# Optimization experiments

Measured on AMD Instinct MI355X. Metric: run time of the kernel, lower is better.

## Reference

```python
import jax, jax.numpy as jnp
import numpy as np

B, T, F_IN = 64, 396, 128
D_MODEL, N_HEAD, D_QKV, D_FF = 768, 8, 96, 3072
N_LAYERS, N_OUT, REL_D = 6, 256, 100


def setup_inputs():
    key = jax.random.key(0)
    cnt = [0]
    def rn(shape, std=1.0):
        cnt[0] += 1
        return jax.random.normal(jax.random.fold_in(key, cnt[0]), shape, jnp.float32) * std
    inp = {"x_raw": rn((B, T, F_IN))}
    def add_rb(p, cin, cout):
        inp[p + "_c1_w"] = rn((cout, cin, 3), (2.0 / (cin * 3)) ** 0.5)
        inp[p + "_c1_b"] = rn((cout,), 0.01)
        inp[p + "_bn1_s"] = 1.0 + rn((cout,), 0.1)
        inp[p + "_bn1_b"] = rn((cout,), 0.1)
        inp[p + "_c2_w"] = rn((cout, cout, 3), (2.0 / (cout * 3)) ** 0.5)
        inp[p + "_c2_b"] = rn((cout,), 0.01)
        inp[p + "_bn2_s"] = 1.0 + rn((cout,), 0.1)
        inp[p + "_bn2_b"] = rn((cout,), 0.1)
        inp[p + "_cr_w"] = rn((cout, cin, 1), (2.0 / cin) ** 0.5)
        inp[p + "_cr_b"] = rn((cout,), 0.01)
        inp[p + "_bnr_s"] = 1.0 + rn((cout,), 0.1)
        inp[p + "_bnr_b"] = rn((cout,), 0.1)
    add_rb("rb1", F_IN, D_MODEL)
    add_rb("rb2", D_MODEL, D_MODEL)
    inp["w_in_w"] = rn((D_MODEL, D_MODEL), D_MODEL ** -0.5)
    inp["w_in_b"] = rn((D_MODEL,), 0.01)
    inp["cls_token"] = jnp.zeros((1, 1, D_MODEL), jnp.float32)
    xav = (2.0 / (D_MODEL + D_QKV)) ** 0.5
    inp["wq"] = rn((N_LAYERS, N_HEAD, D_MODEL, D_QKV), xav)
    inp["wk"] = rn((N_LAYERS, N_HEAD, D_MODEL, D_QKV), xav)
    inp["wv"] = rn((N_LAYERS, N_HEAD, D_MODEL, D_QKV), xav)
    inp["wo"] = rn((N_LAYERS, N_HEAD, D_QKV, D_MODEL), xav)
    inp["rel_emb"] = rn((N_LAYERS, N_HEAD, 2 * REL_D + 1, D_QKV), D_QKV ** -0.5)
    inp["ln1_g"] = jnp.ones((N_LAYERS, D_MODEL), jnp.float32)
    inp["ln1_b"] = jnp.zeros((N_LAYERS, D_MODEL), jnp.float32)
    inp["ln2_g"] = jnp.ones((N_LAYERS, D_MODEL), jnp.float32)
    inp["ln2_b"] = jnp.zeros((N_LAYERS, D_MODEL), jnp.float32)
    inp["ff1_w"] = rn((N_LAYERS, D_FF, D_MODEL), (2.0 / D_MODEL) ** 0.5)
    inp["ff1_b"] = rn((N_LAYERS, D_FF), 0.01)
    inp["ff2_w"] = rn((N_LAYERS, D_MODEL, D_FF), (1.0 / D_FF) ** 0.5)
    inp["ff2_b"] = rn((N_LAYERS, D_MODEL), 0.01)
    inp["w_out_w"] = rn((N_OUT, D_MODEL), D_MODEL ** -0.5)
    inp["w_out_b"] = rn((N_OUT,), 0.01)
    return inp


def _conv1d(x, w, b, stride=1):
    # x: [B, Cin, T], w: [Cout, Cin, K]
    pad = (w.shape[-1] - 1) // 2
    y = jax.lax.conv_general_dilated(x, w, (stride,), [(pad, pad)],
                                     dimension_numbers=("NCH", "OIH", "NCH"))
    return y + b[None, :, None]


def _bn(x, s, b):
    # eval-mode BatchNorm1d folded into per-channel affine
    return x * s[None, :, None] + b[None, :, None]


def _resblock(x, c1w, c1b, s1, b1, c2w, c2b, s2, b2, crw, crb, sr, br, stride):
    h = jax.nn.relu(_bn(_conv1d(x, c1w, c1b, stride), s1, b1))
    h = _bn(_conv1d(h, c2w, c2b), s2, b2)
    r = _bn(_conv1d(x, crw, crb, stride), sr, br)
    return jax.nn.relu(h + r)


def _layer_norm(x, g, b, eps=1e-5):
    m = jnp.mean(x, -1, keepdims=True)
    v = jnp.mean((x - m) ** 2, -1, keepdims=True)
    return (x - m) * jax.lax.rsqrt(v + eps) * g + b


def _attention(x, wq, wk, wv, wo, rel):
    # x: [B, L, D]; relative-positional attention (fairseq LearnedRelativePositionalEmbedding, unmasked)
    L = x.shape[1]
    q = jnp.einsum("btf,hfa->bhta", x, wq) * (D_QKV ** -0.5)
    k = jnp.einsum("btf,hfa->bhta", x, wk)
    v = jnp.einsum("btf,hfa->bhta", x, wv)
    logits = jnp.einsum("bhqa,bhka->bhqk", q, k)
    # narrow embeddings to the 2L-1 relative positions used (L <= REL_D)
    start = REL_D - L
    rel_used = rel[:, start:start + 2 * L - 1, :]  # [h, 2L-1, a]
    pos_all = jnp.einsum("bhqa,hma->bhqm", q, rel_used)  # [B,h,L,2L-1]
    idx = jnp.arange(L)[None, :] - jnp.arange(L)[:, None] + (L - 1)  # [L,L], rel->abs skew
    logits = logits + jnp.take_along_axis(pos_all, idx[None, None], axis=3)
    probs = jax.nn.softmax(logits, axis=-1)
    o = jnp.einsum("bhqk,bhka->bhqa", probs, v)
    return jnp.einsum("bhta,haf->btf", o, wo)


def reference(x_raw, rb1_c1_w, rb1_c1_b, rb1_bn1_s, rb1_bn1_b, rb1_c2_w, rb1_c2_b, rb1_bn2_s, rb1_bn2_b, rb1_cr_w, rb1_cr_b, rb1_bnr_s, rb1_bnr_b, rb2_c1_w, rb2_c1_b, rb2_bn1_s, rb2_bn1_b, rb2_c2_w, rb2_c2_b, rb2_bn2_s, rb2_bn2_b, rb2_cr_w, rb2_cr_b, rb2_bnr_s, rb2_bnr_b, w_in_w, w_in_b, cls_token, wq, wk, wv, wo, rel_emb, ln1_g, ln1_b, ln2_g, ln2_b, ff1_w, ff1_b, ff2_w, ff2_b, w_out_w, w_out_b):
    x = jnp.transpose(x_raw, (0, 2, 1))  # [B, F_IN, T]
    x = _resblock(x, rb1_c1_w, rb1_c1_b, rb1_bn1_s, rb1_bn1_b, rb1_c2_w, rb1_c2_b, rb1_bn2_s, rb1_bn2_b, rb1_cr_w, rb1_cr_b, rb1_bnr_s, rb1_bnr_b, 2)
    x = _resblock(x, rb2_c1_w, rb2_c1_b, rb2_bn1_s, rb2_bn1_b, rb2_c2_w, rb2_c2_b, rb2_bn2_s, rb2_bn2_b, rb2_cr_w, rb2_cr_b, rb2_bnr_s, rb2_bnr_b, 2)
    x = jnp.transpose(x, (0, 2, 1))  # [B, T', D]
    x = x @ w_in_w.T + w_in_b
    cls = jnp.broadcast_to(cls_token, (x.shape[0], 1, D_MODEL))
    x = jnp.concatenate([cls, x], axis=1)  # [B, L, D], L = T'+1
    for l in range(N_LAYERS):
        a = _attention(x, wq[l], wk[l], wv[l], wo[l], rel_emb[l])
        x = _layer_norm(x + a, ln1_g[l], ln1_b[l])
        h = jax.nn.relu(x @ ff1_w[l].T + ff1_b[l]) @ ff2_w[l].T + ff2_b[l]
        x = _layer_norm(x + h, ln2_g[l], ln2_b[l])
    return x[:, 0, :] @ w_out_w.T + w_out_b
```

## Files before the change

kernel.cpp:

```cpp
#include <hip/hip_runtime.h>

typedef _Float16 h8 __attribute__((ext_vector_type(8)));
typedef float f4 __attribute__((ext_vector_type(4)));

namespace {

constexpr int DM   = 768;
constexpr int NHEAD= 8;
constexpr int DQ   = 96;
constexpr int DFF  = 3072;
constexpr int NL   = 6;
constexpr int B_   = 64;
constexpr int T0   = 396, T1 = 198, T2 = 99;
constexpr int FIN  = 128;
constexpr int L_   = 100;
constexpr int MSEQ = B_ * L_;
constexpr int M1   = B_ * T1;
constexpr int M2   = B_ * T2;
constexpr int NREL = 201;
constexpr int POSN = 256;
constexpr int RELK = 128;

enum { EPI_F32 = 0, EPI_RELU_H, EPI_H, EPI_CONV_F32, EPI_CONV_RELU_H, EPI_CONV_ADD_RELU_H };

__device__ __forceinline__ void g2l16(const _Float16* g, _Float16* l)
{
    __builtin_amdgcn_global_load_lds(
        (const __attribute__((address_space(1))) unsigned int*)g,
        (__attribute__((address_space(3))) unsigned int*)l,
        16, 0, 0);
}

template<bool CONV, int EPI, bool OPAD, int MI>
__global__ __launch_bounds__(256)
void gemm5_k(const _Float16* __restrict__ A, const _Float16* __restrict__ B,
             float* __restrict__ Cf, _Float16* __restrict__ Ch,
             const float* __restrict__ bias, const float* __restrict__ bns,
             const float* __restrict__ bnb, const float* __restrict__ res,
             int M, int N, int K, int lda,
             int T_out, int Tp_in, int stride_t, int KS, int in_off,
             int gx, int gxy,
             size_t a_z, size_t b_z, size_t c_z)
{
    constexpr int TM = MI * 32;
    __shared__ _Float16 As[TM * 64];
    __shared__ _Float16 Bs[128 * 64];

    const unsigned nwg = gridDim.x, orig = blockIdx.x;
    const unsigned q = nwg >> 3, rr_ = nwg & 7;
    const unsigned xcd = orig & 7, idx = orig >> 3;
    const unsigned wgid = (xcd < rr_) ? xcd * (q + 1) + idx
                                      : rr_ * (q + 1) + (xcd - rr_) * q + idx;
    const int bz  = (int)(wgid / (unsigned)gxy);
    const int rem = (int)(wgid - (unsigned)bz * (unsigned)gxy);
    const int by  = rem / gx;
    const int bx  = rem - by * gx;

    A += (size_t)bz * a_z;
    B += (size_t)bz * b_z;

    const int tid  = threadIdx.x;
    const int lane = tid & 63;
    const int wid  = tid >> 6;
    const int m0   = by * TM;
    const int n0   = bx * 128;
    const int wm   = (wid >> 1) * (MI * 16);
    const int wn   = (wid & 1) * 64;

    f4 acc[MI][4];
    #pragma unroll
    for (int i = 0; i < MI; ++i)
        #pragma unroll
        for (int j = 0; j < 4; ++j)
            #pragma unroll
            for (int p = 0; p < 4; ++p) acc[i][j][p] = 0.0f;

    const int colh = (((lane & 7) ^ ((lane >> 3) & 7)) << 3);
    size_t aoff[MI];
    #pragma unroll
    for (int i = 0; i < MI; ++i) {
        int m = min(m0 + wid * (MI * 8) + i * 8 + (lane >> 3), M - 1);
        if (CONV) {
            int ab = m / T_out, at = m - ab * T_out;
            aoff[i] = ((size_t)ab * Tp_in + at * stride_t + in_off) * lda + colh;
        } else {
            aoff[i] = (size_t)m * lda + colh;
        }
    }
    size_t boff[4];
    #pragma unroll
    for (int i = 0; i < 4; ++i)
        boff[i] = (size_t)(n0 + wid * 32 + i * 8 + (lane >> 3)) * K + colh;
    const size_t bdk = (size_t)N * K;

    const int fr  = lane & 15;
    const int grp = lane >> 4;

    const int nks = CONV ? KS : 1;
    for (int dk = 0; dk < nks; ++dk) {
        const size_t adk = CONV ? (size_t)dk * lda : 0;
        const size_t bdo = (size_t)dk * bdk;

        for (int k0 = 0; k0 < K; k0 += 64) {
            #pragma unroll
            for (int i = 0; i < MI; ++i)
                g2l16(A + aoff[i] + adk + k0, &As[(wid * (MI * 8) + i * 8) * 64]);
            #pragma unroll
            for (int i = 0; i < 4; ++i)
                g2l16(B + boff[i] + bdo + k0, &Bs[(wid * 32 + i * 8) * 64]);
            __syncthreads();

            #pragma unroll
            for (int kh = 0; kh < 2; ++kh) {
                const int co = (((kh * 4 + grp) ^ (fr & 7)) << 3);
                h8 af[MI], bf[4];
                #pragma unroll
                for (int mi = 0; mi < MI; ++mi)
                    af[mi] = *(const h8*)&As[(wm + mi * 16 + fr) * 64 + co];
                #pragma unroll
                for (int ni = 0; ni < 4; ++ni)
                    bf[ni] = *(const h8*)&Bs[(wn + ni * 16 + fr) * 64 + co];
                #pragma unroll
                for (int mi = 0; mi < MI; ++mi)
                    #pragma unroll
                    for (int ni = 0; ni < 4; ++ni)
                        acc[mi][ni] = __builtin_amdgcn_mfma_f32_16x16x32_f16(
                            af[mi], bf[ni], acc[mi][ni], 0, 0, 0);
            }
            __syncthreads();
        }
    }

    const int frc = lane & 15;
    const int fq4 = (lane >> 4) * 4;
    float*    Cfo = Cf ? Cf + (size_t)bz * c_z : nullptr;
    _Float16* Cho = Ch ? Ch + (size_t)bz * c_z : nullptr;
    #pragma unroll
    for (int mi = 0; mi < MI; ++mi)
        #pragma unroll
        for (int ni = 0; ni < 4; ++ni)
            #pragma unroll
            for (int r = 0; r < 4; ++r) {
                int row = m0 + wm + mi * 16 + fq4 + r;
                int col = n0 + wn + ni * 16 + frc;
                if (row >= M) continue;
                float v = acc[mi][ni][r];
                size_t roff;
                if (OPAD) {
                    int ab = row / T_out, at = row - ab * T_out;
                    roff = ((size_t)ab * (T_out + 2) + at + 1) * N + col;
                } else {
                    roff = (size_t)row * N + col;
                }
                if (EPI == EPI_F32) {
                    if (bias) v += bias[col];
                    Cfo[roff] = v;
                } else if (EPI == EPI_RELU_H) {
                    if (bias) v += bias[col];
                    Cho[roff] = (_Float16)fmaxf(v, 0.0f);
                } else if (EPI == EPI_H) {
                    Cho[roff] = (_Float16)v;
                } else if (EPI == EPI_CONV_F32) {
                    v = bns[col] * (v + bias[col]) + bnb[col];
                    Cfo[roff] = v;
                } else if (EPI == EPI_CONV_RELU_H) {
                    v = bns[col] * (v + bias[col]) + bnb[col];
                    Cho[roff] = (_Float16)fmaxf(v, 0.0f);
                } else {
                    v = bns[col] * (v + bias[col]) + bnb[col] + res[(size_t)row * N + col];
                    Cho[roff] = (_Float16)fmaxf(v, 0.0f);
                }
            }
}


__global__ void f2h_k(const float* __restrict__ in, _Float16* __restrict__ out,
                      long n, float scale)
{
    long i = (long)blockIdx.x * blockDim.x + threadIdx.x;
    if (i < n) out[i] = (_Float16)(in[i] * scale);
}

__global__ void f2h_pad_k(const float* __restrict__ in, _Float16* __restrict__ out)
{
    long i = (long)blockIdx.x * blockDim.x + threadIdx.x;
    if (i >= (long)B_ * 398 * FIN) return;
    int  c = (int)(i % FIN);
    long r = i / FIN;
    int  t = (int)(r % 398);
    int  b = (int)(r / 398);
    float v = (t == 0 || t == 397) ? 0.0f
            : in[((long)b * T0 + (t - 1)) * FIN + c];
    out[i] = (_Float16)v;
}

__global__ void zero_pad_k(_Float16* __restrict__ buf, int Tp, int C)
{
    long i = (long)blockIdx.x * blockDim.x + threadIdx.x;
    if (i >= (long)B_ * 2 * C) return;
    int  c = (int)(i % C);
    long r = i / C;
    int  hi = (int)(r % 2);
    int  b  = (int)(r / 2);
    buf[((size_t)b * Tp + (hi ? Tp - 1 : 0)) * C + c] = (_Float16)0.0f;
}

__global__ void pack_qkv_k(const float* __restrict__ wq, const float* __restrict__ wk,
                           const float* __restrict__ wv, _Float16* __restrict__ out)
{
    long i = (long)blockIdx.x * blockDim.x + threadIdx.x;
    if (i >= (long)NL * 2304 * DM) return;
    int  f = (int)(i % DM);
    long r = i / DM;
    int  n = (int)(r % 2304);
    int  l = (int)(r / 2304);
    int  s = n / DM, hn = n % DM, h = hn / DQ, a = hn % DQ;
    const float* src = (s == 0) ? wq : ((s == 1) ? wk : wv);
    out[i] = (_Float16)src[(((long)l * NHEAD + h) * DM + f) * DQ + a];
}

__global__ void pack_wo_k(const float* __restrict__ wo, _Float16* __restrict__ out)
{
    long i = (long)blockIdx.x * blockDim.x + threadIdx.x;
    if (i >= (long)NL * DM * DM) return;
    int  ha = (int)(i % DM);
    long r  = i / DM;
    int  f  = (int)(r % DM);
    int  l  = (int)(r / DM);
    int  h = ha / DQ, a = ha % DQ;
    out[i] = (_Float16)wo[(((long)l * NHEAD + h) * DQ + a) * DM + f];
}

__global__ void pack_conv_k(const float* __restrict__ w, _Float16* __restrict__ out,
                            int Cout, int Cin, int KS)
{
    long i = (long)blockIdx.x * blockDim.x + threadIdx.x;
    if (i >= (long)Cout * Cin * KS) return;
    int  ci = (int)(i % Cin);
    long r  = i / Cin;
    int  co = (int)(r % Cout);
    int  dk = (int)(r / Cout);
    out[i] = (_Float16)w[((long)co * Cin + ci) * KS + dk];
}

__global__ void pack_rel_k(const float* __restrict__ rel, _Float16* __restrict__ out)
{
    long i = (long)blockIdx.x * blockDim.x + threadIdx.x;
    if (i >= (long)NL * NHEAD * POSN * RELK) return;
    int  k = (int)(i & (RELK - 1));
    long r = i >> 7;
    int  n = (int)(r & (POSN - 1));
    long r2 = r >> 8;
    int  h = (int)(r2 & (NHEAD - 1));
    int  l = (int)(r2 >> 3);
    float v = 0.0f;
    if (n < NREL && k < DQ)
        v = rel[(((long)l * NHEAD + h) * NREL + n) * DQ + k] * 0.10206207261596575f;
    out[i] = (_Float16)v;
}

__global__ void concat_k(const float* __restrict__ xlin, const float* __restrict__ cls,
                         float* __restrict__ xf, _Float16* __restrict__ xh)
{
    long i = (long)blockIdx.x * blockDim.x + threadIdx.x;
    if (i >= (long)MSEQ * DM) return;
    int  c = (int)(i % DM);
    long m = i / DM;
    int  b = (int)(m / L_), t = (int)(m % L_);
    float v = (t == 0) ? cls[c] : xlin[((long)b * (L_ - 1) + (t - 1)) * DM + c];
    xf[i] = v;
    xh[i] = (_Float16)v;
}

__global__ __launch_bounds__(256)
void ln_k(const float* x, const float* __restrict__ d,
          const float* __restrict__ g, const float* __restrict__ bb,
          float* xo, _Float16* __restrict__ xh)
{
    long row = blockIdx.x;
    const float* xr = x + row * DM;
    const float* dr = d + row * DM;
    float v[3];
    float s = 0.0f;
    #pragma unroll
    for (int k = 0; k < 3; ++k) {
        int c = threadIdx.x + 256 * k;
        v[k] = xr[c] + dr[c];
        s += v[k];
    }
    __shared__ float red[8];
    #pragma unroll
    for (int o = 32; o; o >>= 1) s += __shfl_xor(s, o, 64);
    int w = threadIdx.x >> 6, lane = threadIdx.x & 63;
    if (lane == 0) red[w] = s;
    __syncthreads();
    s = red[0] + red[1] + red[2] + red[3];
    float mean = s * (1.0f / DM);
    float vs = 0.0f;
    #pragma unroll
    for (int k = 0; k < 3; ++k) { float t = v[k] - mean; vs += t * t; }
    #pragma unroll
    for (int o = 32; o; o >>= 1) vs += __shfl_xor(vs, o, 64);
    if (lane == 0) red[4 + w] = vs;
    __syncthreads();
    vs = red[4] + red[5] + red[6] + red[7];
    float rstd = rsqrtf(vs * (1.0f / DM) + 1e-5f);
    #pragma unroll
    for (int k = 0; k < 3; ++k) {
        int c = threadIdx.x + 256 * k;
        float y = (v[k] - mean) * rstd * g[c] + bb[c];
        xo[row * DM + c] = y;
        xh[row * DM + c] = (_Float16)y;
    }
}

constexpr int LP = 128;
constexpr int KP = 104;
constexpr int PP = 136;

__global__ __launch_bounds__(256)
void attn_k(const _Float16* __restrict__ qkv, const _Float16* __restrict__ pos,
            _Float16* __restrict__ o)
{
    __shared__ __align__(16) char smem[60928];
    _Float16* Ks = (_Float16*)smem;
    _Float16* Ps = (_Float16*)smem;
    _Float16* Vt = (_Float16*)(smem + 34816);

    const int h = blockIdx.x, b = blockIdx.y;
    const int tid = threadIdx.x, lane = tid & 63, w = tid >> 6;
    const _Float16* base = qkv + (size_t)b * L_ * 2304 + h * DQ;
    const float qscale = 0.10206207261596575f;

    {
        int row = tid >> 1;
        int c0  = (tid & 1) * 48;
        const bool real = row < L_;
        const _Float16* krow = base + 768 + (size_t)row * 2304;
        #pragma unroll
        for (int q = 0; q < 6; ++q) {
            int c = c0 + q * 8;
            h8 kv;
            #pragma unroll
            for (int e = 0; e < 8; ++e) kv[e] = (_Float16)0.0f;
            if (real) kv = *(const h8*)(krow + c);
            *(h8*)&Ks[row * KP + c] = kv;
        }
        for (int idx = tid; idx < DQ * LP; idx += 256) {
            int a = idx % DQ, j = idx / DQ;
            _Float16 v = (_Float16)0.0f;
            if (j < L_) v = base[1536 + (size_t)j * 2304 + a];
            Vt[a * PP + j] = v;
        }
    }
    __syncthreads();

    const int fr = lane & 15;
    const int fk = (lane >> 4) * 8;
    const int rbase = w * 32 + ((lane >> 4) << 2);

    f4 acc[2][8];
    #pragma unroll
    for (int mi = 0; mi < 2; ++mi)
        #pragma unroll
        for (int ni = 0; ni < 8; ++ni)
            #pragma unroll
            for (int q = 0; q < 4; ++q) acc[mi][ni][q] = 0.0f;

    #pragma unroll
    for (int k0 = 0; k0 < DQ; k0 += 32) {
        h8 a0 = *(const h8*)(base + (size_t)(w * 32 + fr) * 2304 + k0 + fk);
        h8 a1 = *(const h8*)(base + (size_t)(w * 32 + 16 + fr) * 2304 + k0 + fk);
        #pragma unroll
        for (int ni = 0; ni < 8; ++ni) {
            h8 bv = *(const h8*)&Ks[(ni * 16 + fr) * KP + k0 + fk];
            acc[0][ni] = __builtin_amdgcn_mfma_f32_16x16x32_f16(a0, bv, acc[0][ni], 0, 0, 0);
            acc[1][ni] = __builtin_amdgcn_mfma_f32_16x16x32_f16(a1, bv, acc[1][ni], 0, 0, 0);
        }
    }

    const _Float16* posb = pos + ((size_t)h * MSEQ + (size_t)b * L_) * POSN;
    #pragma unroll
    for (int mi = 0; mi < 2; ++mi)
        #pragma unroll
        for (int r = 0; r < 4; ++r) {
            int i = rbase + mi * 16 + r;
            float s[8];
            #pragma unroll
            for (int ni = 0; ni < 8; ++ni) {
                int j = ni * 16 + fr;
                float v = -3.0e38f;
                if (i < L_ && j < L_)
                    v = acc[mi][ni][r] * qscale
                      + (float)posb[(size_t)i * POSN + (j - i + (L_ - 1))];
                s[ni] = v;
            }
            float m = s[0];
            #pragma unroll
            for (int ni = 1; ni < 8; ++ni) m = fmaxf(m, s[ni]);
            #pragma unroll
            for (int msk = 1; msk < 16; msk <<= 1) m = fmaxf(m, __shfl_xor(m, msk, 64));
            float sum = 0.0f;
            #pragma unroll
            for (int ni = 0; ni < 8; ++ni) { s[ni] = __expf(s[ni] - m); sum += s[ni]; }
            #pragma unroll
            for (int msk = 1; msk < 16; msk <<= 1) sum += __shfl_xor(sum, msk, 64);
            float inv = 1.0f / sum;
            #pragma unroll
            for (int ni = 0; ni < 8; ++ni) acc[mi][ni][r] = s[ni] * inv;
        }

    __syncthreads();

    #pragma unroll
    for (int mi = 0; mi < 2; ++mi)
        #pragma unroll
        for (int r = 0; r < 4; ++r) {
            int i = rbase + mi * 16 + r;
            #pragma unroll
            for (int ni = 0; ni < 8; ++ni)
                Ps[i * PP + ni * 16 + fr] = (_Float16)acc[mi][ni][r];
        }
    __syncthreads();

    f4 acc2[2][6];
    #pragma unroll
    for (int mi = 0; mi < 2; ++mi)
        #pragma unroll
        for (int ni = 0; ni < 6; ++ni)
            #pragma unroll
            for (int q = 0; q < 4; ++q) acc2[mi][ni][q] = 0.0f;

    #pragma unroll
    for (int k0 = 0; k0 < LP; k0 += 32) {
        h8 a0 = *(const h8*)&Ps[(w * 32 + fr) * PP + k0 + fk];
        h8 a1 = *(const h8*)&Ps[(w * 32 + 16 + fr) * PP + k0 + fk];
        #pragma unroll
        for (int ni = 0; ni < 6; ++ni) {
            h8 bv = *(const h8*)&Vt[(ni * 16 + fr) * PP + k0 + fk];
            acc2[0][ni] = __builtin_amdgcn_mfma_f32_16x16x32_f16(a0, bv, acc2[0][ni], 0, 0, 0);
            acc2[1][ni] = __builtin_amdgcn_mfma_f32_16x16x32_f16(a1, bv, acc2[1][ni], 0, 0, 0);
        }
    }

    _Float16* ob = o + (size_t)b * L_ * DM + h * DQ;
    #pragma unroll
    for (int mi = 0; mi < 2; ++mi)
        #pragma unroll
        for (int r = 0; r < 4; ++r) {
            int i = rbase + mi * 16 + r;
            if (i < L_) {
                #pragma unroll
                for (int ni = 0; ni < 6; ++ni)
                    ob[(size_t)i * DM + ni * 16 + fr] = (_Float16)acc2[mi][ni][r];
            }
        }
}

__global__ __launch_bounds__(256)
void out_k(const float* __restrict__ xseq, const float* __restrict__ w,
           const float* __restrict__ bias, float* __restrict__ out)
{
    __shared__ float xs[DM];
    int b = blockIdx.x;
    for (int c = threadIdx.x; c < DM; c += 256) xs[c] = xseq[(size_t)b * L_ * DM + c];
    __syncthreads();
    int n = threadIdx.x;
    const f4* wr = (const f4*)(w + (size_t)n * DM);
    float acc = 0.0f;
    #pragma unroll 4
    for (int k4 = 0; k4 < DM / 4; ++k4) {
        f4 wv = wr[k4];
        f4 xv = *(const f4*)&xs[k4 * 4];
        acc += wv[0]*xv[0] + wv[1]*xv[1] + wv[2]*xv[2] + wv[3]*xv[3];
    }
    out[(size_t)b * 256 + n] = acc + bias[n];
}

}

extern "C" void kernel_launch(void* const* d_in, const int* in_sizes, int n_in,
                              void* d_out, int out_size, void* d_ws, size_t ws_size,
                              hipStream_t stream)
{
    (void)in_sizes; (void)n_in; (void)out_size; (void)ws_size;

    const float* x_raw   = (const float*)d_in[0];
    const float* rb1_c1w = (const float*)d_in[1];
    const float* rb1_c1b = (const float*)d_in[2];
    const float* rb1_s1  = (const float*)d_in[3];
    const float* rb1_b1  = (const float*)d_in[4];
    const float* rb1_c2w = (const float*)d_in[5];
    const float* rb1_c2b = (const float*)d_in[6];
    const float* rb1_s2  = (const float*)d_in[7];
    const float* rb1_b2  = (const float*)d_in[8];
    const float* rb1_crw = (const float*)d_in[9];
    const float* rb1_crb = (const float*)d_in[10];
    const float* rb1_sr  = (const float*)d_in[11];
    const float* rb1_br  = (const float*)d_in[12];
    const float* rb2_c1w = (const float*)d_in[13];
    const float* rb2_c1b = (const float*)d_in[14];
    const float* rb2_s1  = (const float*)d_in[15];
    const float* rb2_b1  = (const float*)d_in[16];
    const float* rb2_c2w = (const float*)d_in[17];
    const float* rb2_c2b = (const float*)d_in[18];
    const float* rb2_s2  = (const float*)d_in[19];
    const float* rb2_b2  = (const float*)d_in[20];
    const float* rb2_crw = (const float*)d_in[21];
    const float* rb2_crb = (const float*)d_in[22];
    const float* rb2_sr  = (const float*)d_in[23];
    const float* rb2_br  = (const float*)d_in[24];
    const float* w_in_w  = (const float*)d_in[25];
    const float* w_in_b  = (const float*)d_in[26];
    const float* cls     = (const float*)d_in[27];
    const float* wq      = (const float*)d_in[28];
    const float* wk      = (const float*)d_in[29];
    const float* wv      = (const float*)d_in[30];
    const float* wo      = (const float*)d_in[31];
    const float* rel     = (const float*)d_in[32];
    const float* ln1g    = (const float*)d_in[33];
    const float* ln1b    = (const float*)d_in[34];
    const float* ln2g    = (const float*)d_in[35];
    const float* ln2b    = (const float*)d_in[36];
    const float* ff1w    = (const float*)d_in[37];
    const float* ff1b    = (const float*)d_in[38];
    const float* ff2w    = (const float*)d_in[39];
    const float* ff2b    = (const float*)d_in[40];
    const float* w_out_w = (const float*)d_in[41];
    const float* w_out_b = (const float*)d_in[42];

    char* base = (char*)d_ws;
    size_t off = 0;
    auto carve = [&](size_t bytes) -> char* {
        char* p = base + off;
        off = (off + bytes + 255) & ~(size_t)255;
        return p;
    };
    _Float16* w_in_h = (_Float16*)carve((size_t)589824 * 2);
    _Float16* qkvw   = (_Float16*)carve((size_t)10616832 * 2);
    _Float16* wow    = (_Float16*)carve((size_t)3538944 * 2);
    _Float16* ff1h   = (_Float16*)carve((size_t)14155776 * 2);
    _Float16* ff2h   = (_Float16*)carve((size_t)14155776 * 2);
    _Float16* relh   = (_Float16*)carve((size_t)NL * NHEAD * POSN * RELK * 2);
    _Float16* cw11   = (_Float16*)carve((size_t)294912 * 2);
    _Float16* cw12   = (_Float16*)carve((size_t)1769472 * 2);
    _Float16* cw1r   = (_Float16*)carve((size_t)98304 * 2);
    _Float16* cw21   = (_Float16*)carve((size_t)1769472 * 2);
    _Float16* cw22   = (_Float16*)carve((size_t)1769472 * 2);
    _Float16* cw2r   = (_Float16*)carve((size_t)589824 * 2);
    _Float16* xrawp  = (_Float16*)carve((size_t)B_ * 398 * FIN * 2);
    float*    xseq_f = (float*)carve((size_t)4915200 * 4);
    _Float16* xseq_h = (_Float16*)carve((size_t)4915200 * 2);
    _Float16* qkvb   = (_Float16*)carve((size_t)14745600 * 2);
    _Float16* ohb    = (_Float16*)carve((size_t)4915200 * 2);
    float*    af     = (float*)carve((size_t)4915200 * 4);
    char*     hhreg  = carve((size_t)19660800 * 2);
    float*    yf     = (float*)carve((size_t)4915200 * 4);
    _Float16* h1_rb1 = qkvb;
    float*    r_rb1  = (float*)hhreg;
    _Float16* out1   = (_Float16*)af;
    _Float16* h1_rb2 = (_Float16*)xseq_f;
    float*    r_rb2  = yf;
    _Float16* out2   = ohb;
    float*    xlin   = (float*)hhreg;
    _Float16* posh   = (_Float16*)hhreg;
    _Float16* ffh    = (_Float16*)hhreg;

    dim3 blk(256, 1, 1);
    auto grd = [](long n) { return dim3((unsigned)((n + 255) / 256), 1, 1); };
    #define NWG(M, N, TM, GZ) dim3((unsigned)(((N) / 128) * (((M) + (TM) - 1) / (TM)) * (GZ)), 1, 1)
    #define GXY(M, N, TM) ((N) / 128), (((N) / 128) * (((M) + (TM) - 1) / (TM)))

    f2h_pad_k<<<grd((long)B_ * 398 * FIN), blk, 0, stream>>>(x_raw, xrawp);
    zero_pad_k<<<grd((long)B_ * 2 * DM), blk, 0, stream>>>(h1_rb1, 200, DM);
    zero_pad_k<<<grd((long)B_ * 2 * DM), blk, 0, stream>>>(out1, 200, DM);
    zero_pad_k<<<grd((long)B_ * 2 * DM), blk, 0, stream>>>(h1_rb2, 101, DM);
    f2h_k<<<grd(589824), blk, 0, stream>>>(w_in_w, w_in_h, 589824, 1.0f);
    f2h_k<<<grd(14155776), blk, 0, stream>>>(ff1w, ff1h, 14155776, 1.0f);
    f2h_k<<<grd(14155776), blk, 0, stream>>>(ff2w, ff2h, 14155776, 1.0f);
    pack_rel_k<<<grd((long)NL * NHEAD * POSN * RELK), blk, 0, stream>>>(rel, relh);
    pack_qkv_k<<<grd((long)NL * 2304 * DM), blk, 0, stream>>>(wq, wk, wv, qkvw);
    pack_wo_k<<<grd((long)NL * DM * DM), blk, 0, stream>>>(wo, wow);
    pack_conv_k<<<grd(294912), blk, 0, stream>>>(rb1_c1w, cw11, DM, FIN, 3);
    pack_conv_k<<<grd(1769472), blk, 0, stream>>>(rb1_c2w, cw12, DM, DM, 3);
    pack_conv_k<<<grd(98304), blk, 0, stream>>>(rb1_crw, cw1r, DM, FIN, 1);
    pack_conv_k<<<grd(1769472), blk, 0, stream>>>(rb2_c1w, cw21, DM, DM, 3);
    pack_conv_k<<<grd(1769472), blk, 0, stream>>>(rb2_c2w, cw22, DM, DM, 3);
    pack_conv_k<<<grd(589824), blk, 0, stream>>>(rb2_crw, cw2r, DM, DM, 1);

    gemm5_k<true, EPI_CONV_F32, false, 4><<<NWG(M1, DM, 128, 1), blk, 0, stream>>>(
        xrawp, cw1r, r_rb1, nullptr, rb1_crb, rb1_sr, rb1_br, nullptr,
        M1, DM, FIN, FIN, T1, 398, 2, 1, 1, GXY(M1, DM, 128), 0, 0, 0);
    gemm5_k<true, EPI_CONV_RELU_H, true, 4><<<NWG(M1, DM, 128, 1), blk, 0, stream>>>(
        xrawp, cw11, nullptr, h1_rb1, rb1_c1b, rb1_s1, rb1_b1, nullptr,
        M1, DM, FIN, FIN, T1, 398, 2, 3, 0, GXY(M1, DM, 128), 0, 0, 0);
    gemm5_k<true, EPI_CONV_ADD_RELU_H, true, 4><<<NWG(M1, DM, 128, 1), blk, 0, stream>>>(
        h1_rb1, cw12, nullptr, out1, rb1_c2b, rb1_s2, rb1_b2, r_rb1,
        M1, DM, DM, DM, T1, 200, 1, 3, 0, GXY(M1, DM, 128), 0, 0, 0);

    gemm5_k<true, EPI_CONV_F32, false, 2><<<NWG(M2, DM, 64, 1), blk, 0, stream>>>(
        out1, cw2r, r_rb2, nullptr, rb2_crb, rb2_sr, rb2_br, nullptr,
        M2, DM, DM, DM, T2, 200, 2, 1, 1, GXY(M2, DM, 64), 0, 0, 0);
    gemm5_k<true, EPI_CONV_RELU_H, true, 2><<<NWG(M2, DM, 64, 1), blk, 0, stream>>>(
        out1, cw21, nullptr, h1_rb2, rb2_c1b, rb2_s1, rb2_b1, nullptr,
        M2, DM, DM, DM, T2, 200, 2, 3, 0, GXY(M2, DM, 64), 0, 0, 0);
    gemm5_k<true, EPI_CONV_ADD_RELU_H, false, 2><<<NWG(M2, DM, 64, 1), blk, 0, stream>>>(
        h1_rb2, cw22, nullptr, out2, rb2_c2b, rb2_s2, rb2_b2, r_rb2,
        M2, DM, DM, DM, T2, 101, 1, 3, 0, GXY(M2, DM, 64), 0, 0, 0);

    gemm5_k<false, EPI_F32, false, 2><<<NWG(M2, DM, 64, 1), blk, 0, stream>>>(
        out2, w_in_h, xlin, nullptr, w_in_b, nullptr, nullptr, nullptr,
        M2, DM, DM, DM, 0, 0, 0, 0, 0, GXY(M2, DM, 64), 0, 0, 0);
    concat_k<<<grd((long)MSEQ * DM), blk, 0, stream>>>(xlin, cls, xseq_f, xseq_h);

    for (int l = 0; l < NL; ++l) {
        gemm5_k<false, EPI_H, false, 4><<<NWG(MSEQ, 2304, 128, 1), blk, 0, stream>>>(
            xseq_h, qkvw + (size_t)l * 2304 * DM, nullptr, qkvb,
            nullptr, nullptr, nullptr, nullptr,
            MSEQ, 2304, DM, DM, 0, 0, 0, 0, 0, GXY(MSEQ, 2304, 128), 0, 0, 0);
        gemm5_k<false, EPI_H, false, 4><<<NWG(MSEQ, POSN, 128, NHEAD), blk, 0, stream>>>(
            qkvb, relh + (size_t)l * NHEAD * POSN * RELK, nullptr, posh,
            nullptr, nullptr, nullptr, nullptr,
            MSEQ, POSN, RELK, 2304, 0, 0, 0, 0, 0, GXY(MSEQ, POSN, 128),
            (size_t)DQ, (size_t)POSN * RELK, (size_t)MSEQ * POSN);
        attn_k<<<dim3(NHEAD, B_, 1), blk, 0, stream>>>(qkvb, posh, ohb);
        gemm5_k<false, EPI_F32, false, 2><<<NWG(MSEQ, DM, 64, 1), blk, 0, stream>>>(
            ohb, wow + (size_t)l * DM * DM, af, nullptr,
            nullptr, nullptr, nullptr, nullptr,
            MSEQ, DM, DM, DM, 0, 0, 0, 0, 0, GXY(MSEQ, DM, 64), 0, 0, 0);
        ln_k<<<dim3(MSEQ), blk, 0, stream>>>(xseq_f, af, ln1g + l * DM, ln1b + l * DM,
                                             xseq_f, xseq_h);
        gemm5_k<false, EPI_RELU_H, false, 4><<<NWG(MSEQ, DFF, 128, 1), blk, 0, stream>>>(
            xseq_h, ff1h + (size_t)l * DFF * DM, nullptr, ffh,
            ff1b + l * DFF, nullptr, nullptr, nullptr,
            MSEQ, DFF, DM, DM, 0, 0, 0, 0, 0, GXY(MSEQ, DFF, 128), 0, 0, 0);
        gemm5_k<false, EPI_F32, false, 2><<<NWG(MSEQ, DM, 64, 1), blk, 0, stream>>>(
            ffh, ff2h + (size_t)l * DM * DFF, yf, nullptr,
            ff2b + l * DM, nullptr, nullptr, nullptr,
            MSEQ, DM, DFF, DFF, 0, 0, 0, 0, 0, GXY(MSEQ, DM, 64), 0, 0, 0);
        ln_k<<<dim3(MSEQ), blk, 0, stream>>>(xseq_f, yf, ln2g + l * DM, ln2b + l * DM,
                                             xseq_f, xseq_h);
    }

    out_k<<<dim3(B_), blk, 0, stream>>>(xseq_f, w_out_w, w_out_b, (float*)d_out);
    #undef NWG
    #undef GXY
}
```

Before: 2.128 ms.

## Double-buffer LDS tiles in GEMM to overlap global loads with MFMA

```diff
diff --git a/kernel.cpp b/kernel.cpp
--- a/kernel.cpp
+++ b/kernel.cpp
@@ -33,7 +33,7 @@
 
 template<bool CONV, int EPI, bool OPAD, int MI>
 __global__ __launch_bounds__(256)
-void gemm5_k(const _Float16* __restrict__ A, const _Float16* __restrict__ B,
+void gemm6_k(const _Float16* __restrict__ A, const _Float16* __restrict__ B,
              float* __restrict__ Cf, _Float16* __restrict__ Ch,
              const float* __restrict__ bias, const float* __restrict__ bns,
              const float* __restrict__ bnb, const float* __restrict__ res,
@@ -43,8 +43,8 @@
              size_t a_z, size_t b_z, size_t c_z)
 {
     constexpr int TM = MI * 32;
-    __shared__ _Float16 As[TM * 64];
-    __shared__ _Float16 Bs[128 * 64];
+    __shared__ _Float16 As[2][TM * 64];
+    __shared__ _Float16 Bs[2][128 * 64];
 
     const unsigned nwg = gridDim.x, orig = blockIdx.x;
     const unsigned q = nwg >> 3, rr_ = nwg & 7;
@@ -96,39 +96,65 @@
     const int fr  = lane & 15;
     const int grp = lane >> 4;
 
-    const int nks = CONV ? KS : 1;
-    for (int dk = 0; dk < nks; ++dk) {
+    const int ks64 = K >> 6;
+    const int NS   = (CONV ? KS : 1) * ks64;
+
+    auto stage = [&](int step, int buf) {
+        int dk = 0, kk = step;
+        if (CONV) { dk = step / ks64; kk = step - dk * ks64; }
+        const int k0  = kk << 6;
         const size_t adk = CONV ? (size_t)dk * lda : 0;
         const size_t bdo = (size_t)dk * bdk;
-
-        for (int k0 = 0; k0 < K; k0 += 64) {
-            #pragma unroll
-            for (int i = 0; i < MI; ++i)
-                g2l16(A + aoff[i] + adk + k0, &As[(wid * (MI * 8) + i * 8) * 64]);
-            #pragma unroll
-            for (int i = 0; i < 4; ++i)
-                g2l16(B + boff[i] + bdo + k0, &Bs[(wid * 32 + i * 8) * 64]);
-            __syncthreads();
-
-            #pragma unroll
-            for (int kh = 0; kh < 2; ++kh) {
-                const int co = (((kh * 4 + grp) ^ (fr & 7)) << 3);
-                h8 af[MI], bf[4];
-                #pragma unroll
-                for (int mi = 0; mi < MI; ++mi)
-                    af[mi] = *(const h8*)&As[(wm + mi * 16 + fr) * 64 + co];
-                #pragma unroll
-                for (int ni = 0; ni < 4; ++ni)
-                    bf[ni] = *(const h8*)&Bs[(wn + ni * 16 + fr) * 64 + co];
-                #pragma unroll
-                for (int mi = 0; mi < MI; ++mi)
-                    #pragma unroll
-                    for (int ni = 0; ni < 4; ++ni)
-                        acc[mi][ni] = __builtin_amdgcn_mfma_f32_16x16x32_f16(
-                            af[mi], bf[ni], acc[mi][ni], 0, 0, 0);
-            }
-            __syncthreads();
-        }
+        #pragma unroll
+        for (int i = 0; i < MI; ++i)
+            g2l16(A + aoff[i] + adk + k0, &As[buf][(wid * (MI * 8) + i * 8) * 64]);
+        #pragma unroll
+        for (int i = 0; i < 4; ++i)
+            g2l16(B + boff[i] + bdo + k0, &Bs[buf][(wid * 32 + i * 8) * 64]);
+    };
+
+    stage(0, 0);
+    __syncthreads();
+
+    for (int step = 0; step < NS; ++step) {
+        const int cur = step & 1;
+        const _Float16* As_ = As[cur];
+        const _Float16* Bs_ = Bs[cur];
+
+        const int co0 = ((grp ^ (fr & 7)) << 3);
+        h8 af0[MI], bf0[4];
+        #pragma unroll
+        for (int mi = 0; mi < MI; ++mi)
+            af0[mi] = *(const h8*)&As_[(wm + mi * 16 + fr) * 64 + co0];
+        #pragma unroll
+        for (int ni = 0; ni < 4; ++ni)
+            bf0[ni] = *(const h8*)&Bs_[(wn + ni * 16 + fr) * 64 + co0];
+
+        if (step + 1 < NS) stage(step + 1, cur ^ 1);
+
+        #pragma unroll
+        for (int mi = 0; mi < MI; ++mi)
+            #pragma unroll
+            for (int ni = 0; ni < 4; ++ni)
+                acc[mi][ni] = __builtin_amdgcn_mfma_f32_16x16x32_f16(
+                    af0[mi], bf0[ni], acc[mi][ni], 0, 0, 0);
+
+        const int co1 = (((4 + grp) ^ (fr & 7)) << 3);
+        h8 af1[MI], bf1[4];
+        #pragma unroll
+        for (int mi = 0; mi < MI; ++mi)
+            af1[mi] = *(const h8*)&As_[(wm + mi * 16 + fr) * 64 + co1];
+        #pragma unroll
+        for (int ni = 0; ni < 4; ++ni)
+            bf1[ni] = *(const h8*)&Bs_[(wn + ni * 16 + fr) * 64 + co1];
+        #pragma unroll
+        for (int mi = 0; mi < MI; ++mi)
+            #pragma unroll
+            for (int ni = 0; ni < 4; ++ni)
+                acc[mi][ni] = __builtin_amdgcn_mfma_f32_16x16x32_f16(
+                    af1[mi], bf1[ni], acc[mi][ni], 0, 0, 0);
+
+        __syncthreads();
     }
 
     const int frc = lane & 15;
@@ -588,53 +614,53 @@
     pack_conv_k<<<grd(1769472), blk, 0, stream>>>(rb2_c2w, cw22, DM, DM, 3);
     pack_conv_k<<<grd(589824), blk, 0, stream>>>(rb2_crw, cw2r, DM, DM, 1);
 
-    gemm5_k<true, EPI_CONV_F32, false, 4><<<NWG(M1, DM, 128, 1), blk, 0, stream>>>(
+    gemm6_k<true, EPI_CONV_F32, false, 4><<<NWG(M1, DM, 128, 1), blk, 0, stream>>>(
         xrawp, cw1r, r_rb1, nullptr, rb1_crb, rb1_sr, rb1_br, nullptr,
         M1, DM, FIN, FIN, T1, 398, 2, 1, 1, GXY(M1, DM, 128), 0, 0, 0);
-    gemm5_k<true, EPI_CONV_RELU_H, true, 4><<<NWG(M1, DM, 128, 1), blk, 0, stream>>>(
+    gemm6_k<true, EPI_CONV_RELU_H, true, 4><<<NWG(M1, DM, 128, 1), blk, 0, stream>>>(
         xrawp, cw11, nullptr, h1_rb1, rb1_c1b, rb1_s1, rb1_b1, nullptr,
         M1, DM, FIN, FIN, T1, 398, 2, 3, 0, GXY(M1, DM, 128), 0, 0, 0);
-    gemm5_k<true, EPI_CONV_ADD_RELU_H, true, 4><<<NWG(M1, DM, 128, 1), blk, 0, stream>>>(
+    gemm6_k<true, EPI_CONV_ADD_RELU_H, true, 4><<<NWG(M1, DM, 128, 1), blk, 0, stream>>>(
         h1_rb1, cw12, nullptr, out1, rb1_c2b, rb1_s2, rb1_b2, r_rb1,
         M1, DM, DM, DM, T1, 200, 1, 3, 0, GXY(M1, DM, 128), 0, 0, 0);
 
-    gemm5_k<true, EPI_CONV_F32, false, 2><<<NWG(M2, DM, 64, 1), blk, 0, stream>>>(
+    gemm6_k<true, EPI_CONV_F32, false, 2><<<NWG(M2, DM, 64, 1), blk, 0, stream>>>(
         out1, cw2r, r_rb2, nullptr, rb2_crb, rb2_sr, rb2_br, nullptr,
         M2, DM, DM, DM, T2, 200, 2, 1, 1, GXY(M2, DM, 64), 0, 0, 0);
-    gemm5_k<true, EPI_CONV_RELU_H, true, 2><<<NWG(M2, DM, 64, 1), blk, 0, stream>>>(
+    gemm6_k<true, EPI_CONV_RELU_H, true, 2><<<NWG(M2, DM, 64, 1), blk, 0, stream>>>(
         out1, cw21, nullptr, h1_rb2, rb2_c1b, rb2_s1, rb2_b1, nullptr,
         M2, DM, DM, DM, T2, 200, 2, 3, 0, GXY(M2, DM, 64), 0, 0, 0);
-    gemm5_k<true, EPI_CONV_ADD_RELU_H, false, 2><<<NWG(M2, DM, 64, 1), blk, 0, stream>>>(
+    gemm6_k<true, EPI_CONV_ADD_RELU_H, false, 2><<<NWG(M2, DM, 64, 1), blk, 0, stream>>>(
         h1_rb2, cw22, nullptr, out2, rb2_c2b, rb2_s2, rb2_b2, r_rb2,
         M2, DM, DM, DM, T2, 101, 1, 3, 0, GXY(M2, DM, 64), 0, 0, 0);
 
-    gemm5_k<false, EPI_F32, false, 2><<<NWG(M2, DM, 64, 1), blk, 0, stream>>>(
+    gemm6_k<false, EPI_F32, false, 2><<<NWG(M2, DM, 64, 1), blk, 0, stream>>>(
         out2, w_in_h, xlin, nullptr, w_in_b, nullptr, nullptr, nullptr,
         M2, DM, DM, DM, 0, 0, 0, 0, 0, GXY(M2, DM, 64), 0, 0, 0);
     concat_k<<<grd((long)MSEQ * DM), blk, 0, stream>>>(xlin, cls, xseq_f, xseq_h);
 
     for (int l = 0; l < NL; ++l) {
-        gemm5_k<false, EPI_H, false, 4><<<NWG(MSEQ, 2304, 128, 1), blk, 0, stream>>>(
+        gemm6_k<false, EPI_H, false, 4><<<NWG(MSEQ, 2304, 128, 1), blk, 0, stream>>>(
             xseq_h, qkvw + (size_t)l * 2304 * DM, nullptr, qkvb,
             nullptr, nullptr, nullptr, nullptr,
             MSEQ, 2304, DM, DM, 0, 0, 0, 0, 0, GXY(MSEQ, 2304, 128), 0, 0, 0);
-        gemm5_k<false, EPI_H, false, 4><<<NWG(MSEQ, POSN, 128, NHEAD), blk, 0, stream>>>(
+        gemm6_k<false, EPI_H, false, 4><<<NWG(MSEQ, POSN, 128, NHEAD), blk, 0, stream>>>(
             qkvb, relh + (size_t)l * NHEAD * POSN * RELK, nullptr, posh,
             nullptr, nullptr, nullptr, nullptr,
             MSEQ, POSN, RELK, 2304, 0, 0, 0, 0, 0, GXY(MSEQ, POSN, 128),
             (size_t)DQ, (size_t)POSN * RELK, (size_t)MSEQ * POSN);
         attn_k<<<dim3(NHEAD, B_, 1), blk, 0, stream>>>(qkvb, posh, ohb);
-        gemm5_k<false, EPI_F32, false, 2><<<NWG(MSEQ, DM, 64, 1), blk, 0, stream>>>(
+        gemm6_k<false, EPI_F32, false, 2><<<NWG(MSEQ, DM, 64, 1), blk, 0, stream>>>(
             ohb, wow + (size_t)l * DM * DM, af, nullptr,
             nullptr, nullptr, nullptr, nullptr,
             MSEQ, DM, DM, DM, 0, 0, 0, 0, 0, GXY(MSEQ, DM, 64), 0, 0, 0);
         ln_k<<<dim3(MSEQ), blk, 0, stream>>>(xseq_f, af, ln1g + l * DM, ln1b + l * DM,
                                              xseq_f, xseq_h);
-        gemm5_k<false, EPI_RELU_H, false, 4><<<NWG(MSEQ, DFF, 128, 1), blk, 0, stream>>>(
+        gemm6_k<false, EPI_RELU_H, false, 4><<<NWG(MSEQ, DFF, 128, 1), blk, 0, stream>>>(
             xseq_h, ff1h + (size_t)l * DFF * DM, nullptr, ffh,
             ff1b + l * DFF, nullptr, nullptr, nullptr,
             MSEQ, DFF, DM, DM, 0, 0, 0, 0, 0, GXY(MSEQ, DFF, 128), 0, 0, 0);
-        gemm5_k<false, EPI_F32, false, 2><<<NWG(MSEQ, DM, 64, 1), blk, 0, stream>>>(
+        gemm6_k<false, EPI_F32, false, 2><<<NWG(MSEQ, DM, 64, 1), blk, 0, stream>>>(
             ffh, ff2h + (size_t)l * DM * DFF, yf, nullptr,
             ff2b + l * DM, nullptr, nullptr, nullptr,
             MSEQ, DM, DFF, DFF, 0, 0, 0, 0, 0, GXY(MSEQ, DM, 64), 0, 0, 0);
```

After: 2.024 ms (median of 4 runs). 1.05x faster.
